# Kernel optimization log

Measured on AMD Instinct MI355X. Metric: run time of the kernel, lower is better.

The kernel has to match this reference:

```python
import jax, jax.numpy as jnp
import numpy as np

SIG = [1, 1, 1, 1, -1]  # Cl(4,1)
NVEC = 5
GA = 1 << NVEC  # 32


def _build_gp_table():
    # Cayley table for the geometric product on blades indexed by bitmask.
    G = np.zeros((GA, GA, GA), np.float32)
    for a in range(GA):
        for b in range(GA):
            s = 0
            t = a >> 1
            while t:
                s += bin(t & b).count('1')
                t >>= 1
            sign = -1.0 if (s & 1) else 1.0
            common = a & b
            for i in range(NVEC):
                if (common >> i) & 1:
                    sign *= SIG[i]
            G[a, b, a ^ b] = sign
    return G

GP_TABLE = jnp.asarray(_build_gp_table())


def geometric_product(x, y):
    return jnp.einsum('...i,...j,ijk->...k', x, y, GP_TABLE)


def manifold_norm(x):
    # normalize each multivector onto the unit sphere in R^32
    return x / (jnp.linalg.norm(x, axis=-1, keepdims=True) + 1e-6)


def versor_linear(x, W, b):
    # channel mixing shared across multivector components: x [..., in, ga]
    return jnp.einsum('...ig,oi->...og', x, W) + b


def layer_norm2d(x, w, b):
    # LayerNorm over last two dims [D, ga] jointly
    mu = jnp.mean(x, axis=(-2, -1), keepdims=True)
    var = jnp.var(x, axis=(-2, -1), keepdims=True)
    return (x - mu) / jnp.sqrt(var + 1e-5) * w + b


def attention(x, Wq, bq, Wk, bk, Wv, bv, Wo, bo, n_heads):
    B, S, D, G = x.shape
    dh = D // n_heads
    q = versor_linear(x, Wq, bq).reshape(B, S, n_heads, dh, G)
    k = versor_linear(x, Wk, bk).reshape(B, S, n_heads, dh, G)
    v = versor_linear(x, Wv, bv).reshape(B, S, n_heads, dh, G)
    scale = 1.0 / np.sqrt(dh * G).astype(np.float32)
    scores = jnp.einsum('bshdg,bthdg->bhst', q, k) * scale
    probs = jax.nn.softmax(scores, axis=-1)
    o = jnp.einsum('bhst,bthdg->bshdg', probs, v).reshape(B, S, D, G)
    return versor_linear(o, Wo, bo)


N_HEADS = 8


def forward(x, Wq, bq, Wk, bk, Wv, bv, Wo, bo, ln1_w, ln1_b, ln2_w, ln2_b,
            gamma1, gamma2, W1, b1, W2, b2, Wr, br, Wc, bc):
    L = Wq.shape[0]
    for l in range(L):
        h = attention(layer_norm2d(x, ln1_w[l], ln1_b[l]),
                      Wq[l], bq[l], Wk[l], bk[l], Wv[l], bv[l], Wo[l], bo[l], N_HEADS)
        x = manifold_norm(x + gamma1[l] * h)
        m = versor_linear(layer_norm2d(x, ln2_w[l], ln2_b[l]), W1[l], b1[l])
        m = versor_linear(jnp.tanh(m), W2[l], b2[l])
        x = manifold_norm(x + gamma2[l] * m)
    # RecursiveRotorAccumulator: log(S)-step inclusive scan of rotors
    delta = versor_linear(x, Wr, br)
    rot = 0.5 * delta
    rot = rot.at[..., 0].add(1.0)
    rot = manifold_norm(rot)
    S = x.shape[1]
    step = 1
    while step < S:
        left = rot[:, :-step]
        right = rot[:, step:]
        comb = manifold_norm(geometric_product(right, left))
        rot = jnp.concatenate([rot[:, :step], comb], axis=1)
        step *= 2
    pooled = rot[:, -1]  # [B, D, ga]
    logits = pooled.reshape(pooled.shape[0], -1) @ Wc.T + bc
    return logits


def setup_inputs() -> dict:
    key = jax.random.key(0)
    B, S, D, G, L, NC = 8, 256, 64, GA, 4, 1000
    E = 4 * D  # expansion hidden
    ks = jax.random.split(key, 16)
    sd = 0.02
    inp = {
        'x': jax.random.normal(ks[0], (B, S, D, G), jnp.float32),
        'Wq': jax.random.normal(ks[1], (L, D, D), jnp.float32) * sd,
        'bq': jnp.zeros((L, D, G), jnp.float32),
        'Wk': jax.random.normal(ks[2], (L, D, D), jnp.float32) * sd,
        'bk': jnp.zeros((L, D, G), jnp.float32),
        'Wv': jax.random.normal(ks[3], (L, D, D), jnp.float32) * sd,
        'bv': jnp.zeros((L, D, G), jnp.float32),
        'Wo': jax.random.normal(ks[4], (L, D, D), jnp.float32) * sd,
        'bo': jnp.zeros((L, D, G), jnp.float32),
        'ln1_w': jnp.ones((L, D, G), jnp.float32),
        'ln1_b': jnp.zeros((L, D, G), jnp.float32),
        'ln2_w': jnp.ones((L, D, G), jnp.float32),
        'ln2_b': jnp.zeros((L, D, G), jnp.float32),
        'gamma1': 1e-5 * jnp.ones((L, D, G), jnp.float32),
        'gamma2': 1e-5 * jnp.ones((L, D, G), jnp.float32),
        'W1': jax.random.normal(ks[5], (L, E, D), jnp.float32) * sd,
        'b1': jnp.zeros((L, E, G), jnp.float32),
        'W2': jax.random.normal(ks[6], (L, D, E), jnp.float32) * sd,
        'b2': jnp.zeros((L, D, G), jnp.float32),
        'Wr': jax.random.normal(ks[7], (D, D), jnp.float32) * sd,
        'br': jnp.zeros((D, G), jnp.float32),
        'Wc': jax.random.normal(ks[8], (NC, D * G), jnp.float32) * sd,
        'bc': jnp.zeros((NC,), jnp.float32),
    }
    return inp


def reference(x, Wq, bq, Wk, bk, Wv, bv, Wo, bo, ln1_w, ln1_b, ln2_w, ln2_b,
              gamma1, gamma2, W1, b1, W2, b2, Wr, br, Wc, bc):
    return forward(x, Wq, bq, Wk, bk, Wv, bv, Wo, bo, ln1_w, ln1_b, ln2_w, ln2_b,
                   gamma1, gamma2, W1, b1, W2, b2, Wr, br, Wc, bc)
```

## Files before the change

kernel.cpp:

```cpp
#include <hip/hip_runtime.h>
#include <hip/hip_bf16.h>

constexpr int kB  = 8;
constexpr int kS  = 256;
constexpr int kD  = 64;
constexpr int kG  = 32;
constexpr int kE  = 256;
constexpr int kNH = 8;
constexpr int kHD = 256;
constexpr int kDG = kD * kG;
constexpr int kT  = kB * kS;
constexpr int kNC = 1000;

using bf16x8 = __attribute__((ext_vector_type(8))) short;
using f32x4  = __attribute__((ext_vector_type(4))) float;

__device__ __forceinline__ short f2bf(float f) {
    unsigned u = __float_as_uint(f);
    unsigned r = (u + 0x7FFFu + ((u >> 16) & 1u)) >> 16;
    return (short)r;
}

__device__ __forceinline__ float tanh_fast(float x) {
    float a = fabsf(x);
    float e = __expf(-2.f * a);
    float t = (1.f - e) / (1.f + e);
    return copysignf(t, x);
}

__global__ __launch_bounds__(256) void ln_kernel(const float* __restrict__ Xin,
                                                 const float* __restrict__ w,
                                                 const float* __restrict__ b,
                                                 float* __restrict__ A) {
    int t = blockIdx.x, tid = threadIdx.x;
    const float* xp = Xin + (size_t)t * kDG;
    __shared__ float r1[256], r2[256];
    float v[8], s = 0.f, ss = 0.f;
#pragma unroll
    for (int j = 0; j < 8; j++) {
        float x = xp[tid + j * 256];
        v[j] = x; s += x; ss += x * x;
    }
    r1[tid] = s; r2[tid] = ss; __syncthreads();
    for (int o = 128; o > 0; o >>= 1) {
        if (tid < o) { r1[tid] += r1[tid + o]; r2[tid] += r2[tid + o]; }
        __syncthreads();
    }
    float mean = r1[0] * (1.f / kDG);
    float var  = r2[0] * (1.f / kDG) - mean * mean;
    float rstd = rsqrtf(var + 1e-5f);
    float* ao = A + (size_t)t * kDG;
#pragma unroll
    for (int j = 0; j < 8; j++) {
        int jj = tid + j * 256;
        ao[jj] = (v[j] - mean) * rstd * w[jj] + b[jj];
    }
}

__device__ __forceinline__ void epi_res_mn_ln(
    const f32x4 (&acc)[4][2], const float* __restrict__ bias,
    const float* __restrict__ Xin, float* __restrict__ Xout,
    const float* __restrict__ gamma,
    const float* __restrict__ lnw, const float* __restrict__ lnb,
    float* __restrict__ Aout, int tok, int l16, int quad, bool do_ln) {
    const size_t tb = (size_t)tok * kDG;
    float xv[4][2][4];
    float s = 0.f, ss = 0.f;
#pragma unroll
    for (int mt = 0; mt < 4; ++mt)
#pragma unroll
        for (int r = 0; r < 4; ++r) {
            int o = mt * 16 + quad * 4 + r;
            float vv[2]; float sq = 0.f;
#pragma unroll
            for (int nt = 0; nt < 2; ++nt) {
                int g = nt * 16 + l16;
                float h = acc[mt][nt][r] + bias[o * kG + g];
                float v = Xin[tb + o * kG + g] + gamma[o * kG + g] * h;
                vv[nt] = v; sq = fmaf(v, v, sq);
            }
#pragma unroll
            for (int off = 1; off < 16; off <<= 1) sq += __shfl_xor(sq, off, 64);
            float rn = 1.f / (sqrtf(sq) + 1e-6f);
#pragma unroll
            for (int nt = 0; nt < 2; ++nt) {
                int g = nt * 16 + l16;
                float x = vv[nt] * rn;
                xv[mt][nt][r] = x;
                Xout[tb + o * kG + g] = x;
                s += x; ss = fmaf(x, x, ss);
            }
        }
    if (!do_ln) return;
#pragma unroll
    for (int off = 1; off < 64; off <<= 1) {
        s += __shfl_xor(s, off, 64); ss += __shfl_xor(ss, off, 64);
    }
    float mean = s * (1.f / kDG);
    float var  = ss * (1.f / kDG) - mean * mean;
    float rstd = rsqrtf(var + 1e-5f);
#pragma unroll
    for (int mt = 0; mt < 4; ++mt)
#pragma unroll
        for (int nt = 0; nt < 2; ++nt) {
            int g = nt * 16 + l16;
#pragma unroll
            for (int r = 0; r < 4; ++r) {
                int o = mt * 16 + quad * 4 + r;
                Aout[tb + o * kG + g] = (xv[mt][nt][r] - mean) * rstd * lnw[o * kG + g] + lnb[o * kG + g];
            }
        }
}

__global__ __launch_bounds__(256) void vlinT_kernel(const float* __restrict__ X,
                                                    const float* __restrict__ W,
                                                    const float* __restrict__ bias,
                                                    float* __restrict__ OutT) {
    __shared__ float sx[kDG];
    __shared__ float sw[kD * kD];
    int t = blockIdx.x, tid = threadIdx.x;
    const float* xp = X + (size_t)t * kDG;
    for (int j = tid; j < kDG; j += 256) sx[j] = xp[j];
    for (int j = tid; j < kD * kD; j += 256) sw[j] = W[j];
    __syncthreads();
    int g = tid & 31, ob = tid >> 5;
    int b = t >> 8, s = t & 255;
    float* op = OutT + ((size_t)b * kD * kS + s) * kG;
    for (int o = ob; o < kD; o += 8) {
        float acc = bias[o * kG + g];
        const float* wr = sw + o * kD;
#pragma unroll
        for (int i = 0; i < kD; i++) acc += wr[i] * sx[i * kG + g];
        op[(size_t)o * kS * kG + g] = acc;
    }
}

__global__ __launch_bounds__(256, 2) void mlp1_kernel(
    const float* __restrict__ X, const float* __restrict__ W,
    const float* __restrict__ bias, unsigned short* __restrict__ outH) {
    constexpr int M = 256;
    constexpr int WS = 64 + 8;
    __shared__ short sW[M * WS];
    __shared__ short sXT[4][32][WS];

    const int tid = threadIdx.x, wave = tid >> 6, lane = tid & 63;
    const int l16 = lane & 15, quad = lane >> 4;
    const int tok = blockIdx.x * 4 + wave;

    for (int j = tid * 4; j < M * 64; j += 1024) {
        const float4 w4 = *(const float4*)(W + j);
        int o = j >> 6, i = j & 63;
        *(short4*)&sW[o * WS + i] = make_short4(f2bf(w4.x), f2bf(w4.y), f2bf(w4.z), f2bf(w4.w));
    }
    {
        const int g4 = (lane & 7) * 4;
        const int i0 = (lane >> 3) * 8;
        const float* xp = X + (size_t)tok * kDG;
#pragma unroll
        for (int half = 0; half < 2; ++half) {
            float4 vr[4];
#pragma unroll
            for (int r = 0; r < 4; ++r)
                vr[r] = *(const float4*)(xp + (i0 + half * 4 + r) * kG + g4);
#pragma unroll
            for (int gg = 0; gg < 4; ++gg)
                *(short4*)&sXT[wave][g4 + gg][i0 + half * 4] =
                    make_short4(f2bf((&vr[0].x)[gg]), f2bf((&vr[1].x)[gg]),
                                f2bf((&vr[2].x)[gg]), f2bf((&vr[3].x)[gg]));
        }
    }
    __syncthreads();

    bf16x8 bfr[2][2];
#pragma unroll
    for (int c = 0; c < 2; ++c)
#pragma unroll
        for (int nt = 0; nt < 2; ++nt)
            bfr[c][nt] = *(const bf16x8*)&sXT[wave][nt * 16 + l16][c * 32 + quad * 8];

    f32x4 acc[16][2];
#pragma unroll
    for (int mt = 0; mt < 16; ++mt)
#pragma unroll
        for (int nt = 0; nt < 2; ++nt) acc[mt][nt] = (f32x4){0.f, 0.f, 0.f, 0.f};

#pragma unroll
    for (int mt = 0; mt < 16; ++mt)
#pragma unroll
        for (int c = 0; c < 2; ++c) {
            bf16x8 afr = *(const bf16x8*)&sW[(mt * 16 + l16) * WS + c * 32 + quad * 8];
#pragma unroll
            for (int nt = 0; nt < 2; ++nt)
                acc[mt][nt] = __builtin_amdgcn_mfma_f32_16x16x32_bf16(afr, bfr[c][nt], acc[mt][nt], 0, 0, 0);
        }

    unsigned short* op = outH + (size_t)tok * M * kG;
#pragma unroll
    for (int mt = 0; mt < 16; ++mt)
#pragma unroll
        for (int nt = 0; nt < 2; ++nt) {
            int g = nt * 16 + l16;
            int e0 = mt * 16 + quad * 4;
            short4 s4;
            s4.x = f2bf(tanh_fast(acc[mt][nt][0] + bias[(e0 + 0) * kG + g]));
            s4.y = f2bf(tanh_fast(acc[mt][nt][1] + bias[(e0 + 1) * kG + g]));
            s4.z = f2bf(tanh_fast(acc[mt][nt][2] + bias[(e0 + 2) * kG + g]));
            s4.w = f2bf(tanh_fast(acc[mt][nt][3] + bias[(e0 + 3) * kG + g]));
            *(short4*)&op[g * M + e0] = s4;
        }
}

__global__ __launch_bounds__(256, 2) void gemmWo_fused_kernel(
    const float* __restrict__ X, const float* __restrict__ W,
    const float* __restrict__ bias,
    const float* __restrict__ Xin, const float* __restrict__ gamma,
    const float* __restrict__ lnw, const float* __restrict__ lnb,
    float* __restrict__ Xout, float* __restrict__ Aout) {
    constexpr int WS = 64 + 8;
    __shared__ short sW[64 * WS];
    __shared__ short sXT[4][32][WS];

    const int tid = threadIdx.x, wave = tid >> 6, lane = tid & 63;
    const int l16 = lane & 15, quad = lane >> 4;
    const int tok = blockIdx.x * 4 + wave;

    for (int j = tid * 4; j < 64 * 64; j += 1024) {
        const float4 w4 = *(const float4*)(W + j);
        int o = j >> 6, i = j & 63;
        *(short4*)&sW[o * WS + i] = make_short4(f2bf(w4.x), f2bf(w4.y), f2bf(w4.z), f2bf(w4.w));
    }
    {
        const int g4 = (lane & 7) * 4;
        const int i0 = (lane >> 3) * 8;
        const float* xp = X + (size_t)tok * kDG;
#pragma unroll
        for (int half = 0; half < 2; ++half) {
            float4 vr[4];
#pragma unroll
            for (int r = 0; r < 4; ++r)
                vr[r] = *(const float4*)(xp + (i0 + half * 4 + r) * kG + g4);
#pragma unroll
            for (int gg = 0; gg < 4; ++gg)
                *(short4*)&sXT[wave][g4 + gg][i0 + half * 4] =
                    make_short4(f2bf((&vr[0].x)[gg]), f2bf((&vr[1].x)[gg]),
                                f2bf((&vr[2].x)[gg]), f2bf((&vr[3].x)[gg]));
        }
    }
    __syncthreads();

    bf16x8 bfr[2][2];
#pragma unroll
    for (int c = 0; c < 2; ++c)
#pragma unroll
        for (int nt = 0; nt < 2; ++nt)
            bfr[c][nt] = *(const bf16x8*)&sXT[wave][nt * 16 + l16][c * 32 + quad * 8];

    f32x4 acc[4][2];
#pragma unroll
    for (int mt = 0; mt < 4; ++mt)
#pragma unroll
        for (int nt = 0; nt < 2; ++nt) acc[mt][nt] = (f32x4){0.f, 0.f, 0.f, 0.f};

#pragma unroll
    for (int mt = 0; mt < 4; ++mt)
#pragma unroll
        for (int c = 0; c < 2; ++c) {
            bf16x8 afr = *(const bf16x8*)&sW[(mt * 16 + l16) * WS + c * 32 + quad * 8];
#pragma unroll
            for (int nt = 0; nt < 2; ++nt)
                acc[mt][nt] = __builtin_amdgcn_mfma_f32_16x16x32_bf16(afr, bfr[c][nt], acc[mt][nt], 0, 0, 0);
        }

    epi_res_mn_ln(acc, bias, Xin, Xout, gamma, lnw, lnb, Aout, tok, l16, quad, true);
}

__global__ __launch_bounds__(256, 2) void gemm_qkv_kernel(
    const float* __restrict__ X,
    const float* __restrict__ Wq, const float* __restrict__ Wk, const float* __restrict__ Wv,
    const float* __restrict__ bq, const float* __restrict__ bk, const float* __restrict__ bv,
    unsigned short* __restrict__ Q, unsigned short* __restrict__ K, unsigned short* __restrict__ V) {
    constexpr int WS = 64 + 8;
    __shared__ short sW[3 * 64 * WS];
    __shared__ short sXT[4][32][WS];

    const int tid = threadIdx.x, wave = tid >> 6, lane = tid & 63;
    const int l16 = lane & 15, quad = lane >> 4;
    const int tok = blockIdx.x * 4 + wave;

    const float* Wp[3] = {Wq, Wk, Wv};
#pragma unroll
    for (int w = 0; w < 3; ++w)
        for (int j = tid * 4; j < 64 * 64; j += 1024) {
            const float4 w4 = *(const float4*)(Wp[w] + j);
            int o = j >> 6, i = j & 63;
            *(short4*)&sW[w * 64 * WS + o * WS + i] =
                make_short4(f2bf(w4.x), f2bf(w4.y), f2bf(w4.z), f2bf(w4.w));
        }
    {
        const int g4 = (lane & 7) * 4;
        const int i0 = (lane >> 3) * 8;
        const float* xp = X + (size_t)tok * kDG;
#pragma unroll
        for (int half = 0; half < 2; ++half) {
            float4 vr[4];
#pragma unroll
            for (int r = 0; r < 4; ++r)
                vr[r] = *(const float4*)(xp + (i0 + half * 4 + r) * kG + g4);
#pragma unroll
            for (int gg = 0; gg < 4; ++gg)
                *(short4*)&sXT[wave][g4 + gg][i0 + half * 4] =
                    make_short4(f2bf((&vr[0].x)[gg]), f2bf((&vr[1].x)[gg]),
                                f2bf((&vr[2].x)[gg]), f2bf((&vr[3].x)[gg]));
        }
    }
    __syncthreads();

    bf16x8 bfr[2][2];
#pragma unroll
    for (int c = 0; c < 2; ++c)
#pragma unroll
        for (int nt = 0; nt < 2; ++nt)
            bfr[c][nt] = *(const bf16x8*)&sXT[wave][nt * 16 + l16][c * 32 + quad * 8];

    f32x4 acc[3][4][2];
#pragma unroll
    for (int w = 0; w < 3; ++w)
#pragma unroll
        for (int mt = 0; mt < 4; ++mt)
#pragma unroll
            for (int nt = 0; nt < 2; ++nt) acc[w][mt][nt] = (f32x4){0.f, 0.f, 0.f, 0.f};

#pragma unroll
    for (int w = 0; w < 3; ++w)
#pragma unroll
        for (int mt = 0; mt < 4; ++mt)
#pragma unroll
            for (int c = 0; c < 2; ++c) {
                bf16x8 afr = *(const bf16x8*)&sW[w * 64 * WS + (mt * 16 + l16) * WS + c * 32 + quad * 8];
#pragma unroll
                for (int nt = 0; nt < 2; ++nt)
                    acc[w][mt][nt] = __builtin_amdgcn_mfma_f32_16x16x32_bf16(afr, bfr[c][nt], acc[w][mt][nt], 0, 0, 0);
            }

    unsigned short* Op[3] = {Q, K, V};
    const float* Bp[3] = {bq, bk, bv};
#pragma unroll
    for (int w = 0; w < 3; ++w) {
        unsigned short* op = Op[w] + (size_t)tok * kDG;
#pragma unroll
        for (int mt = 0; mt < 4; ++mt)
#pragma unroll
            for (int nt = 0; nt < 2; ++nt) {
                int g = nt * 16 + l16;
#pragma unroll
                for (int r = 0; r < 4; ++r) {
                    int o = mt * 16 + quad * 4 + r;
                    op[o * kG + g] = (unsigned short)f2bf(acc[w][mt][nt][r] + Bp[w][o * kG + g]);
                }
            }
    }
}

template<bool DO_LN>
__global__ __launch_bounds__(256, 2) void mlp2_fused_kernel(
    const unsigned short* __restrict__ Mb,
    const float* __restrict__ W2, const float* __restrict__ b2,
    float* __restrict__ X, const float* __restrict__ gamma,
    const float* __restrict__ lnw, const float* __restrict__ lnb,
    float* __restrict__ Aout) {
    constexpr int WS = 256 + 8;
    __shared__ short sW[64 * WS];
    const int tid = threadIdx.x, wave = tid >> 6, lane = tid & 63;
    const int l16 = lane & 15, quad = lane >> 4;
    const int tok = blockIdx.x * 4 + wave;

    for (int j = tid * 4; j < 64 * 256; j += 1024) {
        const float4 w4 = *(const float4*)(W2 + j);
        int o = j >> 8, i = j & 255;
        *(short4*)&sW[o * WS + i] = make_short4(f2bf(w4.x), f2bf(w4.y), f2bf(w4.z), f2bf(w4.w));
    }
    __syncthreads();

    f32x4 acc[4][2];
#pragma unroll
    for (int mt = 0; mt < 4; ++mt)
#pragma unroll
        for (int nt = 0; nt < 2; ++nt) acc[mt][nt] = (f32x4){0.f, 0.f, 0.f, 0.f};

    const unsigned short* mp = Mb + (size_t)tok * kG * kE;
#pragma unroll
    for (int c = 0; c < 8; ++c) {
        bf16x8 bfr[2];
#pragma unroll
        for (int nt = 0; nt < 2; ++nt)
            bfr[nt] = *(const bf16x8*)&mp[(nt * 16 + l16) * kE + c * 32 + quad * 8];
#pragma unroll
        for (int mt = 0; mt < 4; ++mt) {
            bf16x8 afr = *(const bf16x8*)&sW[(mt * 16 + l16) * WS + c * 32 + quad * 8];
#pragma unroll
            for (int nt = 0; nt < 2; ++nt)
                acc[mt][nt] = __builtin_amdgcn_mfma_f32_16x16x32_bf16(afr, bfr[nt], acc[mt][nt], 0, 0, 0);
        }
    }

    epi_res_mn_ln(acc, b2, X, X, gamma, lnw, lnb, Aout, tok, l16, quad, DO_LN);
}

constexpr int QSTR = 264;
constexpr int VSTR = 40;

__global__ __launch_bounds__(256) void attn_mfma_kernel(const unsigned short* __restrict__ Q,
                                                        const unsigned short* __restrict__ K,
                                                        const unsigned short* __restrict__ V,
                                                        float* __restrict__ O) {
    __shared__ short sQ[64 * QSTR];
    __shared__ short sKV[256 * VSTR];

    const int qt = blockIdx.x, h = blockIdx.y, b = blockIdx.z;
    const int tid = threadIdx.x;
    const int wave = tid >> 6, lane = tid & 63;
    const int l16 = lane & 15, quad = lane >> 4;

    const size_t bh = (size_t)b * kS * kDG + (size_t)h * kHD;

#pragma unroll
    for (int it = 0; it < 8; ++it) {
        int j = it * 2048 + tid * 8;
        int row = j >> 8, col = j & 255;
        *(bf16x8*)&sQ[row * QSTR + col] =
            *(const bf16x8*)(Q + bh + (size_t)(qt * 64 + row) * kDG + col);
    }
    __syncthreads();

    bf16x8 afrag[8];
    {
        int row = wave * 16 + l16;
#pragma unroll
        for (int c = 0; c < 8; ++c)
            afrag[c] = *(const bf16x8*)&sQ[row * QSTR + c * 32 + quad * 8];
    }

    f32x4 acc[16];
#pragma unroll
    for (int i = 0; i < 16; ++i) acc[i] = (f32x4){0.f, 0.f, 0.f, 0.f};

    for (int kt = 0; kt < 8; ++kt) {
        __syncthreads();
#pragma unroll
        for (int it = 0; it < 4; ++it) {
            int j = it * 2048 + tid * 8;
            int row = j >> 8, col = j & 255;
            *(bf16x8*)&sKV[row * QSTR + col] =
                *(const bf16x8*)(K + bh + (size_t)(kt * 32 + row) * kDG + col);
        }
        __syncthreads();
#pragma unroll
        for (int nt = 0; nt < 2; ++nt) {
            int key = nt * 16 + l16;
            f32x4 a = acc[kt * 2 + nt];
#pragma unroll
            for (int c = 0; c < 8; ++c) {
                bf16x8 bfrag = *(const bf16x8*)&sKV[key * QSTR + c * 32 + quad * 8];
                a = __builtin_amdgcn_mfma_f32_16x16x32_bf16(afrag[c], bfrag, a, 0, 0, 0);
            }
            acc[kt * 2 + nt] = a;
        }
    }
    __syncthreads();

    float inv[4];
#pragma unroll
    for (int r = 0; r < 4; ++r) {
        float m = -1e30f;
#pragma unroll
        for (int t = 0; t < 16; ++t) m = fmaxf(m, acc[t][r]);
#pragma unroll
        for (int off = 1; off < 16; off <<= 1) m = fmaxf(m, __shfl_xor(m, off, 16));
        float s = 0.f;
#pragma unroll
        for (int t = 0; t < 16; ++t) {
            float p = __expf((acc[t][r] - m) * 0.0625f);
            acc[t][r] = p; s += p;
        }
#pragma unroll
        for (int off = 1; off < 16; off <<= 1) s += __shfl_xor(s, off, 16);
        inv[r] = 1.f / s;
    }

#pragma unroll
    for (int t = 0; t < 16; ++t)
#pragma unroll
        for (int r = 0; r < 4; ++r)
            sQ[(wave * 16 + quad * 4 + r) * QSTR + t * 16 + l16] = f2bf(acc[t][r]);

    f32x4 oacc[16];
#pragma unroll
    for (int i = 0; i < 16; ++i) oacc[i] = (f32x4){0.f, 0.f, 0.f, 0.f};

    for (int vt = 0; vt < 8; ++vt) {
        __syncthreads();
        {
            int kb = tid >> 5;
#pragma unroll
            for (int it = 0; it < 2; ++it) {
                int db = (tid & 31) + it * 32;
                short4 vr[4];
#pragma unroll
                for (int r = 0; r < 4; ++r)
                    vr[r] = *(const short4*)(V + bh + (size_t)(vt * 32 + kb * 4 + r) * kDG + db * 4);
#pragma unroll
                for (int i = 0; i < 4; ++i) {
                    short4 p = make_short4((&vr[0].x)[i], (&vr[1].x)[i],
                                           (&vr[2].x)[i], (&vr[3].x)[i]);
                    *(short4*)&sKV[(db * 4 + i) * VSTR + kb * 4] = p;
                }
            }
        }
        __syncthreads();
        bf16x8 pfrag = *(const bf16x8*)&sQ[(wave * 16 + l16) * QSTR + vt * 32 + quad * 8];
#pragma unroll
        for (int dt = 0; dt < 16; ++dt) {
            bf16x8 vfrag = *(const bf16x8*)&sKV[(dt * 16 + l16) * VSTR + quad * 8];
            oacc[dt] = __builtin_amdgcn_mfma_f32_16x16x32_bf16(pfrag, vfrag, oacc[dt], 0, 0, 0);
        }
    }

    {
        int qrow = qt * 64 + wave * 16 + quad * 4;
#pragma unroll
        for (int dt = 0; dt < 16; ++dt)
#pragma unroll
            for (int r = 0; r < 4; ++r)
                O[bh + (size_t)(qrow + r) * kDG + dt * 16 + l16] = oacc[dt][r] * inv[r];
    }
}

constexpr int pc_ce(unsigned v) { int c = 0; while (v) { c += v & 1; v >>= 1; } return c; }
constexpr unsigned gp_mask_ce(int a) {
    unsigned m = 0;
    for (int c = 0; c < 32; ++c) {
        int b = a ^ c;
        int s = (a & b) >> 4;
        for (int t = a >> 1; t; t >>= 1) s += pc_ce(t & b);
        if (s & 1) m |= (1u << c);
    }
    return m;
}

template<int A>
__device__ __forceinline__ void gp_term(const float* x, const float* y, float* acc) {
    constexpr unsigned m = gp_mask_ce(A);
    const float xa = x[A], nxa = -xa;
#pragma unroll
    for (int c = 0; c < 32; ++c)
        acc[c] = fmaf(((m >> c) & 1u) ? nxa : xa, y[A ^ c], acc[c]);
}

__device__ __forceinline__ void gp_mn_t(const float* x, const float* y, float* out) {
    float acc[32];
#pragma unroll
    for (int c = 0; c < 32; ++c) acc[c] = 0.f;
    gp_term<0>(x, y, acc);  gp_term<1>(x, y, acc);  gp_term<2>(x, y, acc);  gp_term<3>(x, y, acc);
    gp_term<4>(x, y, acc);  gp_term<5>(x, y, acc);  gp_term<6>(x, y, acc);  gp_term<7>(x, y, acc);
    gp_term<8>(x, y, acc);  gp_term<9>(x, y, acc);  gp_term<10>(x, y, acc); gp_term<11>(x, y, acc);
    gp_term<12>(x, y, acc); gp_term<13>(x, y, acc); gp_term<14>(x, y, acc); gp_term<15>(x, y, acc);
    gp_term<16>(x, y, acc); gp_term<17>(x, y, acc); gp_term<18>(x, y, acc); gp_term<19>(x, y, acc);
    gp_term<20>(x, y, acc); gp_term<21>(x, y, acc); gp_term<22>(x, y, acc); gp_term<23>(x, y, acc);
    gp_term<24>(x, y, acc); gp_term<25>(x, y, acc); gp_term<26>(x, y, acc); gp_term<27>(x, y, acc);
    gp_term<28>(x, y, acc); gp_term<29>(x, y, acc); gp_term<30>(x, y, acc); gp_term<31>(x, y, acc);
    float ss = 0.f;
#pragma unroll
    for (int c = 0; c < 32; ++c) ss = fmaf(acc[c], acc[c], ss);
    float r = 1.f / (sqrtf(ss) + 1e-6f);
#pragma unroll
    for (int c = 0; c < 32; ++c) out[c] = acc[c] * r;
}

__device__ __forceinline__ void leaf_load(const float* base, float* v) {
#pragma unroll
    for (int i = 0; i < 8; ++i) {
        const float4 f = *(const float4*)(base + i * 4);
        v[i * 4 + 0] = 0.5f * f.x; v[i * 4 + 1] = 0.5f * f.y;
        v[i * 4 + 2] = 0.5f * f.z; v[i * 4 + 3] = 0.5f * f.w;
    }
    v[0] += 1.f;
    float ss = 0.f;
#pragma unroll
    for (int c = 0; c < 32; ++c) ss = fmaf(v[c], v[c], ss);
    float r = 1.f / (sqrtf(ss) + 1e-6f);
#pragma unroll
    for (int c = 0; c < 32; ++c) v[c] *= r;
}

__global__ __launch_bounds__(256) void scanreg_kernel(const float* __restrict__ DT,
                                                      float* __restrict__ pooled) {
    const int wave = threadIdx.x >> 6, lane = threadIdx.x & 63;
    const int seq = blockIdx.x * 4 + wave;
    const float* base = DT + ((size_t)seq * kS + lane * 4) * kG;

    float R[32], Y[32], P[32], Xa[32], Yb[32];

    leaf_load(base, R);
    for (int j = 1; j < 4; ++j) {
        leaf_load(base + j * kG, Y);
        gp_mn_t(Y, R, R);
    }

    for (int step = 1; step < 64; step <<= 1) {
        const bool up = lane & step;
#pragma unroll
        for (int c = 0; c < 32; ++c) P[c] = __shfl_xor(R[c], step, 64);
#pragma unroll
        for (int c = 0; c < 32; ++c) {
            Xa[c] = up ? R[c] : P[c];
            Yb[c] = up ? P[c] : R[c];
        }
        gp_mn_t(Xa, Yb, R);
    }

    if (lane == 0) {
        float* op = pooled + (size_t)seq * kG;
#pragma unroll
        for (int i = 0; i < 8; ++i)
            *(float4*)(op + i * 4) = make_float4(R[i * 4], R[i * 4 + 1], R[i * 4 + 2], R[i * 4 + 3]);
    }
}

__global__ __launch_bounds__(256) void cls2_kernel(const float* __restrict__ P,
                                                   const float* __restrict__ Wc,
                                                   const float* __restrict__ bc,
                                                   float* __restrict__ out) {
    __shared__ float sp[kB * kDG];
    const int tid = threadIdx.x, wave = tid >> 6, lane = tid & 63;
    for (int j = tid * 4; j < kB * kDG; j += 1024)
        *(float4*)&sp[j] = *(const float4*)(P + j);
    __syncthreads();

    const int c = blockIdx.x * 4 + wave;
    const float* w = Wc + (size_t)c * kDG;
    float acc[kB];
#pragma unroll
    for (int b = 0; b < kB; ++b) acc[b] = 0.f;
#pragma unroll
    for (int cc = 0; cc < 8; ++cc) {
        const float4 w4 = *(const float4*)(w + cc * 256 + lane * 4);
#pragma unroll
        for (int b = 0; b < kB; ++b) {
            const float4 p4 = *(const float4*)&sp[b * kDG + cc * 256 + lane * 4];
            acc[b] += w4.x * p4.x + w4.y * p4.y + w4.z * p4.z + w4.w * p4.w;
        }
    }
#pragma unroll
    for (int b = 0; b < kB; ++b)
#pragma unroll
        for (int off = 32; off > 0; off >>= 1) acc[b] += __shfl_xor(acc[b], off, 64);
    if (lane == 0) {
        float bias = bc[c];
#pragma unroll
        for (int b = 0; b < kB; ++b) out[b * kNC + c] = acc[b] + bias;
    }
}

extern "C" void kernel_launch(void* const* d_in, const int* in_sizes, int n_in,
                              void* d_out, int out_size, void* d_ws, size_t ws_size,
                              hipStream_t stream) {
    const float* x_in = (const float*)d_in[0];
    const float* Wq   = (const float*)d_in[1];
    const float* bq   = (const float*)d_in[2];
    const float* Wk   = (const float*)d_in[3];
    const float* bk   = (const float*)d_in[4];
    const float* Wv   = (const float*)d_in[5];
    const float* bv   = (const float*)d_in[6];
    const float* Wo   = (const float*)d_in[7];
    const float* bo   = (const float*)d_in[8];
    const float* ln1w = (const float*)d_in[9];
    const float* ln1b = (const float*)d_in[10];
    const float* ln2w = (const float*)d_in[11];
    const float* ln2b = (const float*)d_in[12];
    const float* gm1  = (const float*)d_in[13];
    const float* gm2  = (const float*)d_in[14];
    const float* W1   = (const float*)d_in[15];
    const float* b1   = (const float*)d_in[16];
    const float* W2   = (const float*)d_in[17];
    const float* b2   = (const float*)d_in[18];
    const float* Wr   = (const float*)d_in[19];
    const float* br   = (const float*)d_in[20];
    const float* Wc   = (const float*)d_in[21];
    const float* bc   = (const float*)d_in[22];

    const size_t NEL = (size_t)kT * kDG;
    float* F  = (float*)d_ws;
    float* X  = F;
    float* A  = F + NEL;
    float* Qb = F + 2 * NEL;
    float* Kb = F + 3 * NEL;
    float* Vb = F + 4 * NEL;
    unsigned short* Qh = (unsigned short*)Qb;
    unsigned short* Kh = (unsigned short*)Kb;
    unsigned short* Vh = (unsigned short*)Vb;
    unsigned short* Mb = (unsigned short*)Kb;
    float* pooled = Qb;

    ln_kernel<<<kT, 256, 0, stream>>>(x_in, ln1w, ln1b, A);

    for (int l = 0; l < 4; l++) {
        gemm_qkv_kernel<<<kT / 4, 256, 0, stream>>>(A,
            Wq + l * kD * kD, Wk + l * kD * kD, Wv + l * kD * kD,
            bq + l * kDG, bk + l * kDG, bv + l * kDG, Qh, Kh, Vh);
        attn_mfma_kernel<<<dim3(4, kNH, kB), 256, 0, stream>>>(Qh, Kh, Vh, A);
        gemmWo_fused_kernel<<<kT / 4, 256, 0, stream>>>(A, Wo + l * kD * kD, bo + l * kDG,
            l == 0 ? x_in : X, gm1 + l * kDG, ln2w + l * kDG, ln2b + l * kDG, X, A);
        mlp1_kernel<<<kT / 4, 256, 0, stream>>>(A, W1 + l * kE * kD, b1 + l * kE * kG, Mb);
        if (l < 3)
            mlp2_fused_kernel<true><<<kT / 4, 256, 0, stream>>>(Mb, W2 + l * kD * kE, b2 + l * kDG,
                X, gm2 + l * kDG, ln1w + (l + 1) * kDG, ln1b + (l + 1) * kDG, A);
        else
            mlp2_fused_kernel<false><<<kT / 4, 256, 0, stream>>>(Mb, W2 + l * kD * kE, b2 + l * kDG,
                X, gm2 + l * kDG, nullptr, nullptr, nullptr);
    }

    vlinT_kernel<<<kT, 256, 0, stream>>>(X, Wr, br, A);
    scanreg_kernel<<<kB * kD / 4, 256, 0, stream>>>(A, pooled);
    cls2_kernel<<<kNC / 4, 256, 0, stream>>>(pooled, Wc, bc, (float*)d_out);
}
```

Baseline: 610.6 us.

## Store activations as pre-transposed bf16 and read attention Q/K directly from global

The layer-norm and attention outputs are now written as bf16 in a [token][g][channel] transposed layout. The GEMM kernels can then load MFMA B-fragments straight from global memory instead of reading fp32, converting and transposing through LDS. Attention now loads Q and K fragments directly from global rather than staging them in shared memory, and it transposes its output through LDS so the store is coalesced. This halves activation traffic and removes LDS staging and barriers, at the cost of bf16 rounding on the stored activations and uncached strided global reads for K.

Measured after the change: 752.0 us. +23.1%, slower.

```diff
diff --git a/kernel.cpp b/kernel.cpp
--- a/kernel.cpp
+++ b/kernel.cpp
@@ -28,18 +28,21 @@
     return copysignf(t, x);
 }
 
-__global__ __launch_bounds__(256) void ln_kernel(const float* __restrict__ Xin,
-                                                 const float* __restrict__ w,
-                                                 const float* __restrict__ b,
-                                                 float* __restrict__ A) {
+__global__ __launch_bounds__(256) void lnT_kernel(const float* __restrict__ Xin,
+                                                  const float* __restrict__ w,
+                                                  const float* __restrict__ b,
+                                                  unsigned short* __restrict__ AT) {
     int t = blockIdx.x, tid = threadIdx.x;
+    __shared__ float sv[64 * 33];
+    __shared__ float r1[256], r2[256];
     const float* xp = Xin + (size_t)t * kDG;
-    __shared__ float r1[256], r2[256];
-    float v[8], s = 0.f, ss = 0.f;
+    float s = 0.f, ss = 0.f;
 #pragma unroll
     for (int j = 0; j < 8; j++) {
-        float x = xp[tid + j * 256];
-        v[j] = x; s += x; ss += x * x;
+        int jj = tid + j * 256;
+        float x = xp[jj];
+        sv[(jj >> 5) * 33 + (jj & 31)] = x;
+        s += x; ss += x * x;
     }
     r1[tid] = s; r2[tid] = ss; __syncthreads();
     for (int o = 128; o > 0; o >>= 1) {
@@ -49,12 +52,19 @@
     float mean = r1[0] * (1.f / kDG);
     float var  = r2[0] * (1.f / kDG) - mean * mean;
     float rstd = rsqrtf(var + 1e-5f);
-    float* ao = A + (size_t)t * kDG;
-#pragma unroll
-    for (int j = 0; j < 8; j++) {
-        int jj = tid + j * 256;
-        ao[jj] = (v[j] - mean) * rstd * w[jj] + b[jj];
-    }
+    int g = tid >> 3, i0 = (tid & 7) * 8;
+    short4 o0, o1;
+    short* op = (short*)&o0;
+#pragma unroll
+    for (int k = 0; k < 8; ++k) {
+        int i = i0 + k;
+        float v = sv[i * 33 + g];
+        short r = f2bf((v - mean) * rstd * w[i * kG + g] + b[i * kG + g]);
+        if (k < 4) ((short*)&o0)[k] = r; else ((short*)&o1)[k - 4] = r;
+    }
+    (void)op;
+    *(short4*)&AT[(size_t)t * kDG + g * 64 + i0]     = o0;
+    *(short4*)&AT[(size_t)t * kDG + g * 64 + i0 + 4] = o1;
 }
 
 __device__ __forceinline__ void epi_res_mn_ln(
@@ -62,7 +72,7 @@
     const float* __restrict__ Xin, float* __restrict__ Xout,
     const float* __restrict__ gamma,
     const float* __restrict__ lnw, const float* __restrict__ lnb,
-    float* __restrict__ Aout, int tok, int l16, int quad, bool do_ln) {
+    unsigned short* __restrict__ ATout, int tok, int l16, int quad, bool do_ln) {
     const size_t tb = (size_t)tok * kDG;
     float xv[4][2][4];
     float s = 0.f, ss = 0.f;
@@ -104,11 +114,13 @@
 #pragma unroll
         for (int nt = 0; nt < 2; ++nt) {
             int g = nt * 16 + l16;
+            short4 s4;
 #pragma unroll
             for (int r = 0; r < 4; ++r) {
                 int o = mt * 16 + quad * 4 + r;
-                Aout[tb + o * kG + g] = (xv[mt][nt][r] - mean) * rstd * lnw[o * kG + g] + lnb[o * kG + g];
+                ((short*)&s4)[r] = f2bf((xv[mt][nt][r] - mean) * rstd * lnw[o * kG + g] + lnb[o * kG + g]);
             }
+            *(short4*)&ATout[tb + g * 64 + mt * 16 + quad * 4] = s4;
         }
 }
 
@@ -136,12 +148,11 @@
 }
 
 __global__ __launch_bounds__(256, 2) void mlp1_kernel(
-    const float* __restrict__ X, const float* __restrict__ W,
+    const unsigned short* __restrict__ AT, const float* __restrict__ W,
     const float* __restrict__ bias, unsigned short* __restrict__ outH) {
     constexpr int M = 256;
     constexpr int WS = 64 + 8;
     __shared__ short sW[M * WS];
-    __shared__ short sXT[4][32][WS];
 
     const int tid = threadIdx.x, wave = tid >> 6, lane = tid & 63;
     const int l16 = lane & 15, quad = lane >> 4;
@@ -152,31 +163,16 @@
         int o = j >> 6, i = j & 63;
         *(short4*)&sW[o * WS + i] = make_short4(f2bf(w4.x), f2bf(w4.y), f2bf(w4.z), f2bf(w4.w));
     }
+    bf16x8 bfr[2][2];
     {
-        const int g4 = (lane & 7) * 4;
-        const int i0 = (lane >> 3) * 8;
-        const float* xp = X + (size_t)tok * kDG;
-#pragma unroll
-        for (int half = 0; half < 2; ++half) {
-            float4 vr[4];
-#pragma unroll
-            for (int r = 0; r < 4; ++r)
-                vr[r] = *(const float4*)(xp + (i0 + half * 4 + r) * kG + g4);
-#pragma unroll
-            for (int gg = 0; gg < 4; ++gg)
-                *(short4*)&sXT[wave][g4 + gg][i0 + half * 4] =
-                    make_short4(f2bf((&vr[0].x)[gg]), f2bf((&vr[1].x)[gg]),
-                                f2bf((&vr[2].x)[gg]), f2bf((&vr[3].x)[gg]));
-        }
+        const unsigned short* ap = AT + (size_t)tok * kDG;
+#pragma unroll
+        for (int c = 0; c < 2; ++c)
+#pragma unroll
+            for (int nt = 0; nt < 2; ++nt)
+                bfr[c][nt] = *(const bf16x8*)(ap + (nt * 16 + l16) * 64 + c * 32 + quad * 8);
     }
     __syncthreads();
-
-    bf16x8 bfr[2][2];
-#pragma unroll
-    for (int c = 0; c < 2; ++c)
-#pragma unroll
-        for (int nt = 0; nt < 2; ++nt)
-            bfr[c][nt] = *(const bf16x8*)&sXT[wave][nt * 16 + l16][c * 32 + quad * 8];
 
     f32x4 acc[16][2];
 #pragma unroll
@@ -211,14 +207,13 @@
 }
 
 __global__ __launch_bounds__(256, 2) void gemmWo_fused_kernel(
-    const float* __restrict__ X, const float* __restrict__ W,
+    const unsigned short* __restrict__ AT, const float* __restrict__ W,
     const float* __restrict__ bias,
     const float* __restrict__ Xin, const float* __restrict__ gamma,
     const float* __restrict__ lnw, const float* __restrict__ lnb,
-    float* __restrict__ Xout, float* __restrict__ Aout) {
+    float* __restrict__ Xout, unsigned short* __restrict__ ATout) {
     constexpr int WS = 64 + 8;
     __shared__ short sW[64 * WS];
-    __shared__ short sXT[4][32][WS];
 
     const int tid = threadIdx.x, wave = tid >> 6, lane = tid & 63;
     const int l16 = lane & 15, quad = lane >> 4;
@@ -229,31 +224,16 @@
         int o = j >> 6, i = j & 63;
         *(short4*)&sW[o * WS + i] = make_short4(f2bf(w4.x), f2bf(w4.y), f2bf(w4.z), f2bf(w4.w));
     }
+    bf16x8 bfr[2][2];
     {
-        const int g4 = (lane & 7) * 4;
-        const int i0 = (lane >> 3) * 8;
-        const float* xp = X + (size_t)tok * kDG;
-#pragma unroll
-        for (int half = 0; half < 2; ++half) {
-            float4 vr[4];
-#pragma unroll
-            for (int r = 0; r < 4; ++r)
-                vr[r] = *(const float4*)(xp + (i0 + half * 4 + r) * kG + g4);
-#pragma unroll
-            for (int gg = 0; gg < 4; ++gg)
-                *(short4*)&sXT[wave][g4 + gg][i0 + half * 4] =
-                    make_short4(f2bf((&vr[0].x)[gg]), f2bf((&vr[1].x)[gg]),
-                                f2bf((&vr[2].x)[gg]), f2bf((&vr[3].x)[gg]));
-        }
+        const unsigned short* ap = AT + (size_t)tok * kDG;
+#pragma unroll
+        for (int c = 0; c < 2; ++c)
+#pragma unroll
+            for (int nt = 0; nt < 2; ++nt)
+                bfr[c][nt] = *(const bf16x8*)(ap + (nt * 16 + l16) * 64 + c * 32 + quad * 8);
     }
     __syncthreads();
-
-    bf16x8 bfr[2][2];
-#pragma unroll
-    for (int c = 0; c < 2; ++c)
-#pragma unroll
-        for (int nt = 0; nt < 2; ++nt)
-            bfr[c][nt] = *(const bf16x8*)&sXT[wave][nt * 16 + l16][c * 32 + quad * 8];
 
     f32x4 acc[4][2];
 #pragma unroll
@@ -271,17 +251,16 @@
                 acc[mt][nt] = __builtin_amdgcn_mfma_f32_16x16x32_bf16(afr, bfr[c][nt], acc[mt][nt], 0, 0, 0);
         }
 
-    epi_res_mn_ln(acc, bias, Xin, Xout, gamma, lnw, lnb, Aout, tok, l16, quad, true);
+    epi_res_mn_ln(acc, bias, Xin, Xout, gamma, lnw, lnb, ATout, tok, l16, quad, true);
 }
 
 __global__ __launch_bounds__(256, 2) void gemm_qkv_kernel(
-    const float* __restrict__ X,
+    const unsigned short* __restrict__ AT,
     const float* __restrict__ Wq, const float* __restrict__ Wk, const float* __restrict__ Wv,
     const float* __restrict__ bq, const float* __restrict__ bk, const float* __restrict__ bv,
     unsigned short* __restrict__ Q, unsigned short* __restrict__ K, unsigned short* __restrict__ V) {
     constexpr int WS = 64 + 8;
     __shared__ short sW[3 * 64 * WS];
-    __shared__ short sXT[4][32][WS];
 
     const int tid = threadIdx.x, wave = tid >> 6, lane = tid & 63;
     const int l16 = lane & 15, quad = lane >> 4;
@@ -296,31 +275,16 @@
             *(short4*)&sW[w * 64 * WS + o * WS + i] =
                 make_short4(f2bf(w4.x), f2bf(w4.y), f2bf(w4.z), f2bf(w4.w));
         }
+    bf16x8 bfr[2][2];
     {
-        const int g4 = (lane & 7) * 4;
-        const int i0 = (lane >> 3) * 8;
-        const float* xp = X + (size_t)tok * kDG;
-#pragma unroll
-        for (int half = 0; half < 2; ++half) {
-            float4 vr[4];
-#pragma unroll
-            for (int r = 0; r < 4; ++r)
-                vr[r] = *(const float4*)(xp + (i0 + half * 4 + r) * kG + g4);
-#pragma unroll
-            for (int gg = 0; gg < 4; ++gg)
-                *(short4*)&sXT[wave][g4 + gg][i0 + half * 4] =
-                    make_short4(f2bf((&vr[0].x)[gg]), f2bf((&vr[1].x)[gg]),
-                                f2bf((&vr[2].x)[gg]), f2bf((&vr[3].x)[gg]));
-        }
+        const unsigned short* ap = AT + (size_t)tok * kDG;
+#pragma unroll
+        for (int c = 0; c < 2; ++c)
+#pragma unroll
+            for (int nt = 0; nt < 2; ++nt)
+                bfr[c][nt] = *(const bf16x8*)(ap + (nt * 16 + l16) * 64 + c * 32 + quad * 8);
     }
     __syncthreads();
-
-    bf16x8 bfr[2][2];
-#pragma unroll
-    for (int c = 0; c < 2; ++c)
-#pragma unroll
-        for (int nt = 0; nt < 2; ++nt)
-            bfr[c][nt] = *(const bf16x8*)&sXT[wave][nt * 16 + l16][c * 32 + quad * 8];
 
     f32x4 acc[3][4][2];
 #pragma unroll
@@ -367,7 +331,7 @@
     const float* __restrict__ W2, const float* __restrict__ b2,
     float* __restrict__ X, const float* __restrict__ gamma,
     const float* __restrict__ lnw, const float* __restrict__ lnb,
-    float* __restrict__ Aout) {
+    unsigned short* __restrict__ ATout) {
     constexpr int WS = 256 + 8;
     __shared__ short sW[64 * WS];
     const int tid = threadIdx.x, wave = tid >> 6, lane = tid & 63;
@@ -403,7 +367,7 @@
         }
     }
 
-    epi_res_mn_ln(acc, b2, X, X, gamma, lnw, lnb, Aout, tok, l16, quad, DO_LN);
+    epi_res_mn_ln(acc, b2, X, X, gamma, lnw, lnb, ATout, tok, l16, quad, DO_LN);
 }
 
 constexpr int QSTR = 264;
@@ -412,9 +376,9 @@
 __global__ __launch_bounds__(256) void attn_mfma_kernel(const unsigned short* __restrict__ Q,
                                                         const unsigned short* __restrict__ K,
                                                         const unsigned short* __restrict__ V,
-                                                        float* __restrict__ O) {
-    __shared__ short sQ[64 * QSTR];
-    __shared__ short sKV[256 * VSTR];
+                                                        unsigned short* __restrict__ AT) {
+    __shared__ short sP[64 * QSTR];
+    __shared__ short sVT[256 * VSTR];
 
     const int qt = blockIdx.x, h = blockIdx.y, b = blockIdx.z;
     const int tid = threadIdx.x;
@@ -423,50 +387,28 @@
 
     const size_t bh = (size_t)b * kS * kDG + (size_t)h * kHD;
 
-#pragma unroll
-    for (int it = 0; it < 8; ++it) {
-        int j = it * 2048 + tid * 8;
-        int row = j >> 8, col = j & 255;
-        *(bf16x8*)&sQ[row * QSTR + col] =
-            *(const bf16x8*)(Q + bh + (size_t)(qt * 64 + row) * kDG + col);
-    }
-    __syncthreads();
-
     bf16x8 afrag[8];
     {
-        int row = wave * 16 + l16;
+        const unsigned short* qp = Q + bh + (size_t)(qt * 64 + wave * 16 + l16) * kDG;
 #pragma unroll
         for (int c = 0; c < 8; ++c)
-            afrag[c] = *(const bf16x8*)&sQ[row * QSTR + c * 32 + quad * 8];
+            afrag[c] = *(const bf16x8*)(qp + c * 32 + quad * 8);
     }
 
     f32x4 acc[16];
 #pragma unroll
     for (int i = 0; i < 16; ++i) acc[i] = (f32x4){0.f, 0.f, 0.f, 0.f};
-
-    for (int kt = 0; kt < 8; ++kt) {
-        __syncthreads();
-#pragma unroll
-        for (int it = 0; it < 4; ++it) {
-            int j = it * 2048 + tid * 8;
-            int row = j >> 8, col = j & 255;
-            *(bf16x8*)&sKV[row * QSTR + col] =
-                *(const bf16x8*)(K + bh + (size_t)(kt * 32 + row) * kDG + col);
-        }
-        __syncthreads();
-#pragma unroll
-        for (int nt = 0; nt < 2; ++nt) {
-            int key = nt * 16 + l16;
-            f32x4 a = acc[kt * 2 + nt];
-#pragma unroll
-            for (int c = 0; c < 8; ++c) {
-                bf16x8 bfrag = *(const bf16x8*)&sKV[key * QSTR + c * 32 + quad * 8];
-                a = __builtin_amdgcn_mfma_f32_16x16x32_bf16(afrag[c], bfrag, a, 0, 0, 0);
-            }
-            acc[kt * 2 + nt] = a;
-        }
-    }
-    __syncthreads();
+#pragma unroll 2
+    for (int n = 0; n < 16; ++n) {
+        const unsigned short* kp = K + bh + (size_t)(n * 16 + l16) * kDG;
+        f32x4 a = acc[n];
+#pragma unroll
+        for (int c = 0; c < 8; ++c) {
+            bf16x8 bfrag = *(const bf16x8*)(kp + c * 32 + quad * 8);
+            a = __builtin_amdgcn_mfma_f32_16x16x32_bf16(afrag[c], bfrag, a, 0, 0, 0);
+        }
+        acc[n] = a;
+    }
 
     float inv[4];
 #pragma unroll
@@ -491,7 +433,7 @@
     for (int t = 0; t < 16; ++t)
 #pragma unroll
         for (int r = 0; r < 4; ++r)
-            sQ[(wave * 16 + quad * 4 + r) * QSTR + t * 16 + l16] = f2bf(acc[t][r]);
+            sP[(wave * 16 + quad * 4 + r) * QSTR + t * 16 + l16] = f2bf(acc[t][r]);
 
     f32x4 oacc[16];
 #pragma unroll
@@ -512,26 +454,34 @@
                 for (int i = 0; i < 4; ++i) {
                     short4 p = make_short4((&vr[0].x)[i], (&vr[1].x)[i],
                                            (&vr[2].x)[i], (&vr[3].x)[i]);
-                    *(short4*)&sKV[(db * 4 + i) * VSTR + kb * 4] = p;
+                    *(short4*)&sVT[(db * 4 + i) * VSTR + kb * 4] = p;
                 }
             }
         }
         __syncthreads();
-        bf16x8 pfrag = *(const bf16x8*)&sQ[(wave * 16 + l16) * QSTR + vt * 32 + quad * 8];
+        bf16x8 pfrag = *(const bf16x8*)&sP[(wave * 16 + l16) * QSTR + vt * 32 + quad * 8];
 #pragma unroll
         for (int dt = 0; dt < 16; ++dt) {
-            bf16x8 vfrag = *(const bf16x8*)&sKV[(dt * 16 + l16) * VSTR + quad * 8];
+            bf16x8 vfrag = *(const bf16x8*)&sVT[(dt * 16 + l16) * VSTR + quad * 8];
             oacc[dt] = __builtin_amdgcn_mfma_f32_16x16x32_bf16(pfrag, vfrag, oacc[dt], 0, 0, 0);
         }
     }
 
-    {
-        int qrow = qt * 64 + wave * 16 + quad * 4;
-#pragma unroll
-        for (int dt = 0; dt < 16; ++dt)
-#pragma unroll
-            for (int r = 0; r < 4; ++r)
-                O[bh + (size_t)(qrow + r) * kDG + dt * 16 + l16] = oacc[dt][r] * inv[r];
+#pragma unroll
+    for (int dt = 0; dt < 16; ++dt)
+#pragma unroll
+        for (int r = 0; r < 4; ++r) {
+            int hd = dt * 16 + l16;
+            int g = hd & 31, il = hd >> 5;
+            sP[(wave * 16 + quad * 4 + r) * QSTR + g * 8 + il] = f2bf(oacc[dt][r] * inv[r]);
+        }
+    __syncthreads();
+#pragma unroll
+    for (int it = 0; it < 8; ++it) {
+        int idx = it * 256 + tid;
+        int q = idx >> 5, g = idx & 31;
+        size_t dst = ((size_t)(b * kS + qt * 64 + q)) * kDG + g * 64 + h * 8;
+        *(bf16x8*)&AT[dst] = *(const bf16x8*)&sP[q * QSTR + g * 8];
     }
 }
 
@@ -691,35 +641,33 @@
     const size_t NEL = (size_t)kT * kDG;
     float* F  = (float*)d_ws;
     float* X  = F;
-    float* A  = F + NEL;
-    float* Qb = F + 2 * NEL;
-    float* Kb = F + 3 * NEL;
-    float* Vb = F + 4 * NEL;
-    unsigned short* Qh = (unsigned short*)Qb;
-    unsigned short* Kh = (unsigned short*)Kb;
-    unsigned short* Vh = (unsigned short*)Vb;
-    unsigned short* Mb = (unsigned short*)Kb;
-    float* pooled = Qb;
-
-    ln_kernel<<<kT, 256, 0, stream>>>(x_in, ln1w, ln1b, A);
+    unsigned short* Ah = (unsigned short*)(F + NEL);
+    float* DT = F + NEL;
+    unsigned short* Qh = (unsigned short*)(F + 2 * NEL);
+    unsigned short* Kh = (unsigned short*)(F + 3 * NEL);
+    unsigned short* Vh = (unsigned short*)(F + 4 * NEL);
+    unsigned short* Mb = (unsigned short*)(F + 3 * NEL);
+    float* pooled = F + 2 * NEL;
+
+    lnT_kernel<<<kT, 256, 0, stream>>>(x_in, ln1w, ln1b, Ah);
 
     for (int l = 0; l < 4; l++) {
-        gemm_qkv_kernel<<<kT / 4, 256, 0, stream>>>(A,
+        gemm_qkv_kernel<<<kT / 4, 256, 0, stream>>>(Ah,
             Wq + l * kD * kD, Wk + l * kD * kD, Wv + l * kD * kD,
             bq + l * kDG, bk + l * kDG, bv + l * kDG, Qh, Kh, Vh);
-        attn_mfma_kernel<<<dim3(4, kNH, kB), 256, 0, stream>>>(Qh, Kh, Vh, A);
-        gemmWo_fused_kernel<<<kT / 4, 256, 0, stream>>>(A, Wo + l * kD * kD, bo + l * kDG,
-            l == 0 ? x_in : X, gm1 + l * kDG, ln2w + l * kDG, ln2b + l * kDG, X, A);
-        mlp1_kernel<<<kT / 4, 256, 0, stream>>>(A, W1 + l * kE * kD, b1 + l * kE * kG, Mb);
+        attn_mfma_kernel<<<dim3(4, kNH, kB), 256, 0, stream>>>(Qh, Kh, Vh, Ah);
+        gemmWo_fused_kernel<<<kT / 4, 256, 0, stream>>>(Ah, Wo + l * kD * kD, bo + l * kDG,
+            l == 0 ? x_in : X, gm1 + l * kDG, ln2w + l * kDG, ln2b + l * kDG, X, Ah);
+        mlp1_kernel<<<kT / 4, 256, 0, stream>>>(Ah, W1 + l * kE * kD, b1 + l * kE * kG, Mb);
         if (l < 3)
             mlp2_fused_kernel<true><<<kT / 4, 256, 0, stream>>>(Mb, W2 + l * kD * kE, b2 + l * kDG,
-                X, gm2 + l * kDG, ln1w + (l + 1) * kDG, ln1b + (l + 1) * kDG, A);
+                X, gm2 + l * kDG, ln1w + (l + 1) * kDG, ln1b + (l + 1) * kDG, Ah);
         else
             mlp2_fused_kernel<false><<<kT / 4, 256, 0, stream>>>(Mb, W2 + l * kD * kE, b2 + l * kDG,
                 X, gm2 + l * kDG, nullptr, nullptr, nullptr);
     }
 
-    vlinT_kernel<<<kT, 256, 0, stream>>>(X, Wr, br, A);
-    scanreg_kernel<<<kB * kD / 4, 256, 0, stream>>>(A, pooled);
+    vlinT_kernel<<<kT, 256, 0, stream>>>(X, Wr, br, DT);
+    scanreg_kernel<<<kB * kD / 4, 256, 0, stream>>>(DT, pooled);
     cls2_kernel<<<kNC / 4, 256, 0, stream>>>(pooled, Wc, bc, (float*)d_out);
 }
```
